# Kernel tuning notes

Measured on AMD Instinct MI355X. Metric: run time of the kernel, lower is better.

The kernel has to match this reference:

```python
import jax, jax.numpy as jnp
import numpy as np

B, S, H = 1, 1024, 2048
E, I, TOP_K = 64, 768, 8


def setup_inputs() -> dict:
    key = jax.random.key(0)
    k1, k2, k3, k4, k5 = jax.random.split(key, 5)
    std = 0.02
    return {
        "hidden_states": jax.random.normal(k1, (B, S, H), dtype=jnp.float32),
        "router_w": jax.random.normal(k2, (E, H), dtype=jnp.float32) * std,
        "gate_w": jax.random.normal(k3, (E, I, H), dtype=jnp.float32) * std,
        "up_w": jax.random.normal(k4, (E, I, H), dtype=jnp.float32) * std,
        "down_w": jax.random.normal(k5, (E, H, I), dtype=jnp.float32) * std,
    }


def reference(hidden_states, router_w, gate_w, up_w, down_w):
    b, s, h = hidden_states.shape
    x = hidden_states.reshape(-1, h)                     # [T, H]
    T = x.shape[0]

    # Router: softmax in fp32, top-k, renormalize (matches torch source).
    logits = x @ router_w.T                              # [T, E]
    probs = jax.nn.softmax(logits.astype(jnp.float32), axis=-1)
    topk_w, topk_idx = jax.lax.top_k(probs, TOP_K)       # [T, K]
    topk_w = topk_w / jnp.sum(topk_w, axis=-1, keepdims=True)
    topk_w = topk_w.astype(hidden_states.dtype)

    # Dense combine weights: zero for unselected experts. [T, E]
    tok = jnp.arange(T)[:, None]
    combine = jnp.zeros((T, E), dtype=hidden_states.dtype).at[tok, topk_idx].add(topk_w)

    # Scan over experts: SwiGLU MLP on all tokens, weighted-accumulate.
    # Tokens with zero combine weight contribute nothing (same math as the
    # gather/scatter loop in the torch source).
    def body(acc, p):
        gw, uw, dw, cw = p                                # [I,H],[I,H],[H,I],[T]
        hidden = jax.nn.silu(x @ gw.T) * (x @ uw.T)       # [T, I]
        out = hidden @ dw.T                               # [T, H]
        return acc + cw[:, None] * out, None

    init = jnp.zeros_like(x)
    final, _ = jax.lax.scan(body, init, (gate_w, up_w, down_w, combine.T))
    return final.reshape(b, s, h)
```

## Files before the change

kernel.cpp:

```cpp
#include <hip/hip_runtime.h>

#define T_TOK 1024
#define HD    2048
#define NE    64
#define ID    768
#define TOPK  8

typedef __bf16 bf16x8 __attribute__((ext_vector_type(8)));
typedef float  f32x4  __attribute__((ext_vector_type(4)));

#define LGKM0  asm volatile("s_waitcnt lgkmcnt(0)" ::: "memory")
#define VMC(N) asm volatile("s_waitcnt vmcnt(" N ")" ::: "memory")
#define BAR()  __builtin_amdgcn_s_barrier()
#define SCHED0 __builtin_amdgcn_sched_barrier(0)
#define FENCE  asm volatile("" ::: "memory")

__device__ __forceinline__ void load_lds16(const void* src, void* lds) {
  __builtin_amdgcn_global_load_lds(
      (const __attribute__((address_space(1))) void*)src,
      (__attribute__((address_space(3))) void*)lds, 16, 0, 0);
}

__device__ __forceinline__ bf16x8 cvt8(f32x4 a, f32x4 b) {
  bf16x8 r;
  #pragma unroll
  for (int j = 0; j < 4; ++j) { r[j] = (__bf16)a[j]; r[j + 4] = (__bf16)b[j]; }
  return r;
}

__global__ __launch_bounds__(256) void router_kernel(
    const float* __restrict__ x, const float* __restrict__ rw,
    unsigned short* __restrict__ xb_u, float* __restrict__ tw,
    int* __restrict__ counts, int* __restrict__ lists)
{
  __shared__ float  sx[HD];
  __shared__ double slog[NE];
  const int t = blockIdx.x;
  const int tid = threadIdx.x;
  __bf16* xb = (__bf16*)xb_u;

  for (int i = tid; i < HD; i += 256) {
    float v = x[(size_t)t * HD + i];
    sx[i] = v;
    xb[(size_t)t * HD + i] = (__bf16)v;
  }
  __syncthreads();

  const int e = tid >> 2, p = tid & 3;
  const float* rwrow = rw + (size_t)e * HD;
  double acc = 0.0;
  for (int k = p; k < HD; k += 4)
    acc += (double)sx[k] * (double)rwrow[k];
  acc += __shfl_xor(acc, 1, 64);
  acc += __shfl_xor(acc, 2, 64);
  if (p == 0) slog[e] = acc;
  __syncthreads();

  if (tid < 64) {
    double v = slog[tid];
    double selv = -1e300; int seli = 0; double gmax = 0.0;
    #pragma unroll
    for (int k = 0; k < TOPK; ++k) {
      double bv = v; int bi = tid;
      #pragma unroll
      for (int off = 32; off >= 1; off >>= 1) {
        double ov = __shfl_xor(bv, off, 64);
        int    oi = __shfl_xor(bi, off, 64);
        if (ov > bv || (ov == bv && oi < bi)) { bv = ov; bi = oi; }
      }
      if (k == 0) gmax = bv;
      if (tid == k) { selv = bv; seli = bi; }
      if (tid == bi) v = -1e300;
    }
    double e_ = (tid < TOPK) ? exp(selv - gmax) : 0.0;
    double s = e_;
    #pragma unroll
    for (int off = 32; off >= 1; off >>= 1) s += __shfl_xor(s, off, 64);
    if (tid < TOPK) {
      int slot = t * TOPK + tid;
      tw[slot] = (float)(e_ / s);
      int pos = atomicAdd(&counts[seli], 1);
      lists[seli * T_TOK + pos] = slot;
    }
  }
}

__global__ __launch_bounds__(512, 2) void gemm1_kernel(
    const unsigned short* __restrict__ xb_u,
    const float* __restrict__ gw, const float* __restrict__ uw,
    const int* __restrict__ counts, const int* __restrict__ lists,
    unsigned short* __restrict__ hb_u)
{
  __shared__ __bf16 sA[2][24576];
  __shared__ int    sSlot[192];

  const char* xbp = (const char*)xb_u;
  __bf16* hb = (__bf16*)hb_u;
  char* sAc = (char*)&sA[0][0];

  const int wg  = blockIdx.x;
  const int idx = wg >> 3;
  const int e   = (wg & 7) * 8 + idx / 12;
  const int n0  = (idx % 12) * 64;
  const int tid = threadIdx.x, wid = tid >> 6, lane = tid & 63;
  const int n_e = counts[e];
  const int isu = wid >> 2;

  const char* wlane = (const char*)(isu ? uw : gw)
      + ((size_t)e * ID + n0 + (wid & 3) * 16 + (lane & 15)) * (size_t)(HD * 4)
      + (size_t)(lane >> 4) * 32;

#define ISSUE_A1(BUFB, KC)                                                      \
  { char* dst_ = sAc + (BUFB) * 49152 + wid * 6144;                             \
    _Pragma("unroll") for (int j = 0; j < 6; ++j)                               \
      load_lds16(aAddr[j] + (KC) * 256, dst_ + j * 1024); }                     \
  FENCE;

#define ISSUE_W1(NXT, KC)                                                       \
  _Pragma("unroll") for (int p = 0; p < 8; ++p)                                 \
    NXT[p] = *(const f32x4*)(wlane + (size_t)(KC) * 512 + (p >> 1) * 128 + (p & 1) * 16); \
  FENCE;

#define COMP1(CUR, BUFB)                                                        \
  { const char* rb_ = sAc + (BUFB) * 49152;                                     \
    bf16x8 bf_[4];                                                              \
    _Pragma("unroll") for (int ks = 0; ks < 4; ++ks)                            \
      bf_[ks] = cvt8(CUR[2 * ks], CUR[2 * ks + 1]);                             \
    _Pragma("unroll") for (int ks = 0; ks < 4; ++ks) {                          \
      const int K_ = ks * 4 + (lane >> 4);                                      \
      _Pragma("unroll") for (int g = 0; g < 12; ++g) if (g * 16 < rem) {        \
        const int tok_ = g * 16 + (lane & 15);                                  \
        bf16x8 aF_ = *(const bf16x8*)(rb_ + tok_ * 256 + ((K_ ^ (tok_ & 7)) << 4)); \
        acc[g] = __builtin_amdgcn_mfma_f32_16x16x32_bf16(aF_, bf_[ks], acc[g], 0, 0, 0); } } }

#define STEP1(KC, CUR, NXT)                                                     \
  ISSUE_A1(((KC) + 1) & 1, (KC) + 1)                                            \
  ISSUE_W1(NXT, (KC) + 1)                                                       \
  COMP1(CUR, (KC) & 1)                                                          \
  LGKM0; SCHED0; VMC("8"); BAR();

  for (int m0 = 0; m0 < n_e; m0 += 192) {
    __syncthreads();
    if (tid < 192) sSlot[tid] = (m0 + tid < n_e) ? lists[e * T_TOK + m0 + tid] : 0;
    __syncthreads();
    const int rem = (n_e - m0 < 192) ? (n_e - m0) : 192;

    const char* aAddr[6];
    #pragma unroll
    for (int j = 0; j < 6; ++j) {
      int tok = wid * 24 + j * 4 + (lane >> 4);
      int sl = sSlot[tok];
      aAddr[j] = xbp + (size_t)(sl >> 3) * 4096 + (((lane & 15) ^ (tok & 7)) << 4);
    }

    f32x4 acc[12];
    #pragma unroll
    for (int g = 0; g < 12; ++g) acc[g] = (f32x4){0.f, 0.f, 0.f, 0.f};
    f32x4 wA[8], wB[8];

    ISSUE_A1(0, 0)
    ISSUE_W1(wA, 0)
    VMC("8"); BAR();

    #pragma unroll 1
    for (int it = 0; it < 7; ++it) {
      STEP1(2 * it,     wA, wB)
      STEP1(2 * it + 1, wB, wA)
    }
    STEP1(14, wA, wB)
    COMP1(wB, 1)

    if (isu) {
      #pragma unroll
      for (int g = 0; g < 12; ++g) if (g * 16 < rem)
        #pragma unroll
        for (int j = 0; j < 4; ++j) {
          int tok = g * 16 + (lane >> 4) * 4 + j;
          int cl = (wid & 3) * 16 + (lane & 15);
          *(float*)(sAc + tok * 256 + ((cl ^ ((tok & 3) << 4)) << 2)) = acc[g][j];
        }
    }
    __syncthreads();
    if (!isu) {
      #pragma unroll
      for (int g = 0; g < 12; ++g) if (g * 16 < rem)
        #pragma unroll
        for (int j = 0; j < 4; ++j) {
          int tok = g * 16 + (lane >> 4) * 4 + j;
          if (tok < rem) {
            int cl = (wid & 3) * 16 + (lane & 15);
            float uv = *(const float*)(sAc + tok * 256 + ((cl ^ ((tok & 3) << 4)) << 2));
            float gv = acc[g][j];
            int s = sSlot[tok];
            float hv = (gv / (1.0f + expf(-gv))) * uv;
            hb[(size_t)s * ID + (size_t)(n0 + cl)] = (__bf16)hv;
          }
        }
    }
    __syncthreads();
  }
#undef STEP1
#undef COMP1
#undef ISSUE_W1
#undef ISSUE_A1
}

__global__ __launch_bounds__(512, 2) void gemm2_kernel(
    const unsigned short* __restrict__ hb_u,
    const float* __restrict__ dw,
    const int* __restrict__ counts, const int* __restrict__ lists,
    const float* __restrict__ tw,
    float* __restrict__ out)
{
  __shared__ __bf16 sA[2][24576];
  __shared__ int    sSlot[192];

  const char* hbp = (const char*)hb_u;
  char* sAc = (char*)&sA[0][0];

  const int wg  = blockIdx.x;
  const int idx = wg >> 3;
  const int e   = (wg & 7) * 8 + idx / 16;
  const int n0  = (idx % 16) * 128;
  const int tid = threadIdx.x, wid = tid >> 6, lane = tid & 63;
  const int n_e = counts[e];

  const char* wlane = (const char*)dw
      + ((size_t)e * HD + n0 + wid * 16 + (lane & 15)) * (size_t)(ID * 4)
      + (size_t)(lane >> 4) * 32;

#define ISSUE_A2(BUFB, KC)                                                      \
  { char* dst_ = sAc + (BUFB) * 49152 + wid * 6144;                             \
    _Pragma("unroll") for (int j = 0; j < 6; ++j)                               \
      load_lds16(aAddr[j] + (KC) * 256, dst_ + j * 1024); }                     \
  FENCE;

#define ISSUE_W2(NXT, KC)                                                       \
  _Pragma("unroll") for (int p = 0; p < 8; ++p)                                 \
    NXT[p] = *(const f32x4*)(wlane + (size_t)(KC) * 512 + (p >> 1) * 128 + (p & 1) * 16); \
  FENCE;

#define COMP2(CUR, BUFB)                                                        \
  { const char* rb_ = sAc + (BUFB) * 49152;                                     \
    bf16x8 bf_[4];                                                              \
    _Pragma("unroll") for (int ks = 0; ks < 4; ++ks)                            \
      bf_[ks] = cvt8(CUR[2 * ks], CUR[2 * ks + 1]);                             \
    _Pragma("unroll") for (int ks = 0; ks < 4; ++ks) {                          \
      const int K_ = ks * 4 + (lane >> 4);                                      \
      _Pragma("unroll") for (int g = 0; g < 12; ++g) if (g * 16 < rem) {        \
        const int tok_ = g * 16 + (lane & 15);                                  \
        bf16x8 aF_ = *(const bf16x8*)(rb_ + tok_ * 256 + ((K_ ^ (tok_ & 7)) << 4)); \
        acc[g] = __builtin_amdgcn_mfma_f32_16x16x32_bf16(aF_, bf_[ks], acc[g], 0, 0, 0); } } }

#define STEP2(KC, CUR, NXT)                                                     \
  ISSUE_A2(((KC) + 1) & 1, (KC) + 1)                                            \
  ISSUE_W2(NXT, (KC) + 1)                                                       \
  COMP2(CUR, (KC) & 1)                                                          \
  LGKM0; SCHED0; VMC("8"); BAR();

  for (int m0 = 0; m0 < n_e; m0 += 192) {
    __syncthreads();
    if (tid < 192) sSlot[tid] = (m0 + tid < n_e) ? lists[e * T_TOK + m0 + tid] : 0;
    __syncthreads();
    const int rem = (n_e - m0 < 192) ? (n_e - m0) : 192;

    const char* aAddr[6];
    #pragma unroll
    for (int j = 0; j < 6; ++j) {
      int tok = wid * 24 + j * 4 + (lane >> 4);
      int sl = sSlot[tok];
      aAddr[j] = hbp + (size_t)sl * 1536 + (((lane & 15) ^ (tok & 7)) << 4);
    }

    f32x4 acc[12];
    #pragma unroll
    for (int g = 0; g < 12; ++g) acc[g] = (f32x4){0.f, 0.f, 0.f, 0.f};
    f32x4 wA[8], wB[8];

    ISSUE_A2(0, 0)
    ISSUE_W2(wA, 0)
    VMC("8"); BAR();

    #pragma unroll 1
    for (int it = 0; it < 2; ++it) {
      STEP2(2 * it,     wA, wB)
      STEP2(2 * it + 1, wB, wA)
    }
    STEP2(4, wA, wB)
    COMP2(wB, 1)

    #pragma unroll
    for (int g = 0; g < 12; ++g) if (g * 16 < rem)
      #pragma unroll
      for (int j = 0; j < 4; ++j) {
        int tok = g * 16 + (lane >> 4) * 4 + j;
        if (tok < rem) {
          int s = sSlot[tok];
          float w = tw[s];
          atomicAdd(out + (size_t)(s >> 3) * HD + (size_t)(n0 + wid * 16 + (lane & 15)),
                    w * acc[g][j]);
        }
      }
  }
#undef STEP2
#undef COMP2
#undef ISSUE_W2
#undef ISSUE_A2
}

extern "C" void kernel_launch(void* const* d_in, const int* in_sizes, int n_in,
                              void* d_out, int out_size, void* d_ws, size_t ws_size,
                              hipStream_t stream) {
  const float* x  = (const float*)d_in[0];
  const float* rw = (const float*)d_in[1];
  const float* gw = (const float*)d_in[2];
  const float* uw = (const float*)d_in[3];
  const float* dw = (const float*)d_in[4];
  float* out = (float*)d_out;

  char* ws = (char*)d_ws;
  const size_t XB_OFF  = 0;
  const size_t TW_OFF  = XB_OFF + (size_t)T_TOK * HD * 2;
  const size_t CNT_OFF = TW_OFF + (size_t)T_TOK * TOPK * 4;
  const size_t LST_OFF = CNT_OFF + 256;
  const size_t HB_OFF  = LST_OFF + (size_t)NE * T_TOK * 4;

  unsigned short* xb  = (unsigned short*)(ws + XB_OFF);
  float*          tw  = (float*)(ws + TW_OFF);
  int*            cnt = (int*)(ws + CNT_OFF);
  int*            lst = (int*)(ws + LST_OFF);
  unsigned short* hb  = (unsigned short*)(ws + HB_OFF);

  hipMemsetAsync(cnt, 0, 256, stream);
  hipMemsetAsync(d_out, 0, (size_t)T_TOK * HD * sizeof(float), stream);

  router_kernel<<<T_TOK, 256, 0, stream>>>(x, rw, xb, tw, cnt, lst);
  gemm1_kernel<<<768, 512, 0, stream>>>(xb, gw, uw, cnt, lst, hb);
  gemm2_kernel<<<1024, 512, 0, stream>>>(hb, dw, cnt, lst, tw, out);
}
```

Baseline: 516.9 us.

## Halve K-chunk per pipeline stage to cut LDS and registers for higher occupancy

Both expert GEMM kernels now process a 64-wide K chunk per step instead of 128, halving the double-buffered LDS tile and the per-lane weight register buffers. Launch bounds are raised from 2 to 4 blocks per CU to exploit the smaller footprint. The K loop runs twice as many steps, each with its own barrier and waitcnt, and the final step drains with vmcnt(0). This trades more synchronisation per unit of work for more resident waves to hide global load latency.

```diff
diff --git a/kernel.cpp b/kernel.cpp
--- a/kernel.cpp
+++ b/kernel.cpp
@@ -9,7 +9,6 @@
 typedef __bf16 bf16x8 __attribute__((ext_vector_type(8)));
 typedef float  f32x4  __attribute__((ext_vector_type(4)));
 
-#define LGKM0  asm volatile("s_waitcnt lgkmcnt(0)" ::: "memory")
 #define VMC(N) asm volatile("s_waitcnt vmcnt(" N ")" ::: "memory")
 #define BAR()  __builtin_amdgcn_s_barrier()
 #define SCHED0 __builtin_amdgcn_sched_barrier(0)
@@ -85,13 +84,13 @@
   }
 }
 
-__global__ __launch_bounds__(512, 2) void gemm1_kernel(
+__global__ __launch_bounds__(512, 4) void gemm1_kernel(
     const unsigned short* __restrict__ xb_u,
     const float* __restrict__ gw, const float* __restrict__ uw,
     const int* __restrict__ counts, const int* __restrict__ lists,
     unsigned short* __restrict__ hb_u)
 {
-  __shared__ __bf16 sA[2][24576];
+  __shared__ __bf16 sA[2][12288];
   __shared__ int    sSlot[192];
 
   const char* xbp = (const char*)xb_u;
@@ -110,34 +109,35 @@
       + ((size_t)e * ID + n0 + (wid & 3) * 16 + (lane & 15)) * (size_t)(HD * 4)
       + (size_t)(lane >> 4) * 32;
 
-#define ISSUE_A1(BUFB, KC)                                                      \
-  { char* dst_ = sAc + (BUFB) * 49152 + wid * 6144;                             \
-    _Pragma("unroll") for (int j = 0; j < 6; ++j)                               \
-      load_lds16(aAddr[j] + (KC) * 256, dst_ + j * 1024); }                     \
-  FENCE;
-
-#define ISSUE_W1(NXT, KC)                                                       \
-  _Pragma("unroll") for (int p = 0; p < 8; ++p)                                 \
-    NXT[p] = *(const f32x4*)(wlane + (size_t)(KC) * 512 + (p >> 1) * 128 + (p & 1) * 16); \
-  FENCE;
-
-#define COMP1(CUR, BUFB)                                                        \
-  { const char* rb_ = sAc + (BUFB) * 49152;                                     \
-    bf16x8 bf_[4];                                                              \
-    _Pragma("unroll") for (int ks = 0; ks < 4; ++ks)                            \
-      bf_[ks] = cvt8(CUR[2 * ks], CUR[2 * ks + 1]);                             \
-    _Pragma("unroll") for (int ks = 0; ks < 4; ++ks) {                          \
-      const int K_ = ks * 4 + (lane >> 4);                                      \
+#define STEP1(BUFC, CUR, NXT, KN, DOI)                                          \
+  {                                                                             \
+    if (DOI) {                                                                  \
+      char* d_ = sAc + (1 - (BUFC)) * 24576 + wid * 3072;                       \
+      load_lds16(aA0 + (size_t)(KN) * 128, d_);                                 \
+      load_lds16(aA1 + (size_t)(KN) * 128, d_ + 1024);                          \
+      load_lds16(aA2 + (size_t)(KN) * 128, d_ + 2048);                          \
+      NXT[0] = *(const f32x4*)(wlane + (size_t)(KN) * 256);                     \
+      NXT[1] = *(const f32x4*)(wlane + (size_t)(KN) * 256 + 16);                \
+      NXT[2] = *(const f32x4*)(wlane + (size_t)(KN) * 256 + 128);               \
+      NXT[3] = *(const f32x4*)(wlane + (size_t)(KN) * 256 + 144);               \
+    }                                                                           \
+    FENCE;                                                                      \
+    {                                                                           \
+      const char* rb_ = sAc + (BUFC) * 24576;                                   \
+      bf16x8 bw0_ = cvt8(CUR[0], CUR[1]);                                       \
+      bf16x8 bw1_ = cvt8(CUR[2], CUR[3]);                                       \
+      const int c0_ = (lane >> 4), c1_ = 4 + (lane >> 4);                       \
       _Pragma("unroll") for (int g = 0; g < 12; ++g) if (g * 16 < rem) {        \
         const int tok_ = g * 16 + (lane & 15);                                  \
-        bf16x8 aF_ = *(const bf16x8*)(rb_ + tok_ * 256 + ((K_ ^ (tok_ & 7)) << 4)); \
-        acc[g] = __builtin_amdgcn_mfma_f32_16x16x32_bf16(aF_, bf_[ks], acc[g], 0, 0, 0); } } }
-
-#define STEP1(KC, CUR, NXT)                                                     \
-  ISSUE_A1(((KC) + 1) & 1, (KC) + 1)                                            \
-  ISSUE_W1(NXT, (KC) + 1)                                                       \
-  COMP1(CUR, (KC) & 1)                                                          \
-  LGKM0; SCHED0; VMC("8"); BAR();
+        bf16x8 a0_ = *(const bf16x8*)(rb_ + tok_ * 128 + ((c0_ ^ (tok_ & 7)) << 4)); \
+        acc[g] = __builtin_amdgcn_mfma_f32_16x16x32_bf16(a0_, bw0_, acc[g], 0, 0, 0); \
+        bf16x8 a1_ = *(const bf16x8*)(rb_ + tok_ * 128 + ((c1_ ^ (tok_ & 7)) << 4)); \
+        acc[g] = __builtin_amdgcn_mfma_f32_16x16x32_bf16(a1_, bw1_, acc[g], 0, 0, 0); \
+      }                                                                         \
+    }                                                                           \
+    if (DOI) { VMC("4"); } else { VMC("0"); }                                   \
+    BAR(); SCHED0;                                                              \
+  }
 
   for (int m0 = 0; m0 < n_e; m0 += 192) {
     __syncthreads();
@@ -145,30 +145,37 @@
     __syncthreads();
     const int rem = (n_e - m0 < 192) ? (n_e - m0) : 192;
 
-    const char* aAddr[6];
-    #pragma unroll
-    for (int j = 0; j < 6; ++j) {
-      int tok = wid * 24 + j * 4 + (lane >> 4);
-      int sl = sSlot[tok];
-      aAddr[j] = xbp + (size_t)(sl >> 3) * 4096 + (((lane & 15) ^ (tok & 7)) << 4);
-    }
+    const int r0 = wid * 24 + (lane >> 3);
+    const int r1 = r0 + 8, r2 = r0 + 16;
+    const char* aA0 = xbp + (size_t)(sSlot[r0] >> 3) * 4096 + (((lane & 7) ^ (r0 & 7)) << 4);
+    const char* aA1 = xbp + (size_t)(sSlot[r1] >> 3) * 4096 + (((lane & 7) ^ (r1 & 7)) << 4);
+    const char* aA2 = xbp + (size_t)(sSlot[r2] >> 3) * 4096 + (((lane & 7) ^ (r2 & 7)) << 4);
 
     f32x4 acc[12];
     #pragma unroll
     for (int g = 0; g < 12; ++g) acc[g] = (f32x4){0.f, 0.f, 0.f, 0.f};
-    f32x4 wA[8], wB[8];
-
-    ISSUE_A1(0, 0)
-    ISSUE_W1(wA, 0)
-    VMC("8"); BAR();
+    f32x4 wA[4], wB[4];
+
+    {
+      char* d_ = sAc + wid * 3072;
+      load_lds16(aA0, d_);
+      load_lds16(aA1, d_ + 1024);
+      load_lds16(aA2, d_ + 2048);
+      wA[0] = *(const f32x4*)(wlane);
+      wA[1] = *(const f32x4*)(wlane + 16);
+      wA[2] = *(const f32x4*)(wlane + 128);
+      wA[3] = *(const f32x4*)(wlane + 144);
+    }
+    FENCE;
+    VMC("4"); BAR(); SCHED0;
 
     #pragma unroll 1
-    for (int it = 0; it < 7; ++it) {
-      STEP1(2 * it,     wA, wB)
-      STEP1(2 * it + 1, wB, wA)
-    }
-    STEP1(14, wA, wB)
-    COMP1(wB, 1)
+    for (int it = 0; it < 15; ++it) {
+      STEP1(0, wA, wB, 2 * it + 1, 1)
+      STEP1(1, wB, wA, 2 * it + 2, 1)
+    }
+    STEP1(0, wA, wB, 31, 1)
+    STEP1(1, wB, wA, 0, 0)
 
     if (isu) {
       #pragma unroll
@@ -200,19 +207,16 @@
     __syncthreads();
   }
 #undef STEP1
-#undef COMP1
-#undef ISSUE_W1
-#undef ISSUE_A1
-}
-
-__global__ __launch_bounds__(512, 2) void gemm2_kernel(
+}
+
+__global__ __launch_bounds__(512, 4) void gemm2_kernel(
     const unsigned short* __restrict__ hb_u,
     const float* __restrict__ dw,
     const int* __restrict__ counts, const int* __restrict__ lists,
     const float* __restrict__ tw,
     float* __restrict__ out)
 {
-  __shared__ __bf16 sA[2][24576];
+  __shared__ __bf16 sA[2][12288];
   __shared__ int    sSlot[192];
 
   const char* hbp = (const char*)hb_u;
@@ -229,34 +233,35 @@
       + ((size_t)e * HD + n0 + wid * 16 + (lane & 15)) * (size_t)(ID * 4)
       + (size_t)(lane >> 4) * 32;
 
-#define ISSUE_A2(BUFB, KC)                                                      \
-  { char* dst_ = sAc + (BUFB) * 49152 + wid * 6144;                             \
-    _Pragma("unroll") for (int j = 0; j < 6; ++j)                               \
-      load_lds16(aAddr[j] + (KC) * 256, dst_ + j * 1024); }                     \
-  FENCE;
-
-#define ISSUE_W2(NXT, KC)                                                       \
-  _Pragma("unroll") for (int p = 0; p < 8; ++p)                                 \
-    NXT[p] = *(const f32x4*)(wlane + (size_t)(KC) * 512 + (p >> 1) * 128 + (p & 1) * 16); \
-  FENCE;
-
-#define COMP2(CUR, BUFB)                                                        \
-  { const char* rb_ = sAc + (BUFB) * 49152;                                     \
-    bf16x8 bf_[4];                                                              \
-    _Pragma("unroll") for (int ks = 0; ks < 4; ++ks)                            \
-      bf_[ks] = cvt8(CUR[2 * ks], CUR[2 * ks + 1]);                             \
-    _Pragma("unroll") for (int ks = 0; ks < 4; ++ks) {                          \
-      const int K_ = ks * 4 + (lane >> 4);                                      \
+#define STEP2(BUFC, CUR, NXT, KN, DOI)                                          \
+  {                                                                             \
+    if (DOI) {                                                                  \
+      char* d_ = sAc + (1 - (BUFC)) * 24576 + wid * 3072;                       \
+      load_lds16(aA0 + (size_t)(KN) * 128, d_);                                 \
+      load_lds16(aA1 + (size_t)(KN) * 128, d_ + 1024);                          \
+      load_lds16(aA2 + (size_t)(KN) * 128, d_ + 2048);                          \
+      NXT[0] = *(const f32x4*)(wlane + (size_t)(KN) * 256);                     \
+      NXT[1] = *(const f32x4*)(wlane + (size_t)(KN) * 256 + 16);                \
+      NXT[2] = *(const f32x4*)(wlane + (size_t)(KN) * 256 + 128);               \
+      NXT[3] = *(const f32x4*)(wlane + (size_t)(KN) * 256 + 144);               \
+    }                                                                           \
+    FENCE;                                                                      \
+    {                                                                           \
+      const char* rb_ = sAc + (BUFC) * 24576;                                   \
+      bf16x8 bw0_ = cvt8(CUR[0], CUR[1]);                                       \
+      bf16x8 bw1_ = cvt8(CUR[2], CUR[3]);                                       \
+      const int c0_ = (lane >> 4), c1_ = 4 + (lane >> 4);                       \
       _Pragma("unroll") for (int g = 0; g < 12; ++g) if (g * 16 < rem) {        \
         const int tok_ = g * 16 + (lane & 15);                                  \
-        bf16x8 aF_ = *(const bf16x8*)(rb_ + tok_ * 256 + ((K_ ^ (tok_ & 7)) << 4)); \
-        acc[g] = __builtin_amdgcn_mfma_f32_16x16x32_bf16(aF_, bf_[ks], acc[g], 0, 0, 0); } } }
-
-#define STEP2(KC, CUR, NXT)                                                     \
-  ISSUE_A2(((KC) + 1) & 1, (KC) + 1)                                            \
-  ISSUE_W2(NXT, (KC) + 1)                                                       \
-  COMP2(CUR, (KC) & 1)                                                          \
-  LGKM0; SCHED0; VMC("8"); BAR();
+        bf16x8 a0_ = *(const bf16x8*)(rb_ + tok_ * 128 + ((c0_ ^ (tok_ & 7)) << 4)); \
+        acc[g] = __builtin_amdgcn_mfma_f32_16x16x32_bf16(a0_, bw0_, acc[g], 0, 0, 0); \
+        bf16x8 a1_ = *(const bf16x8*)(rb_ + tok_ * 128 + ((c1_ ^ (tok_ & 7)) << 4)); \
+        acc[g] = __builtin_amdgcn_mfma_f32_16x16x32_bf16(a1_, bw1_, acc[g], 0, 0, 0); \
+      }                                                                         \
+    }                                                                           \
+    if (DOI) { VMC("4"); } else { VMC("0"); }                                   \
+    BAR(); SCHED0;                                                              \
+  }
 
   for (int m0 = 0; m0 < n_e; m0 += 192) {
     __syncthreads();
@@ -264,30 +269,37 @@
     __syncthreads();
     const int rem = (n_e - m0 < 192) ? (n_e - m0) : 192;
 
-    const char* aAddr[6];
-    #pragma unroll
-    for (int j = 0; j < 6; ++j) {
-      int tok = wid * 24 + j * 4 + (lane >> 4);
-      int sl = sSlot[tok];
-      aAddr[j] = hbp + (size_t)sl * 1536 + (((lane & 15) ^ (tok & 7)) << 4);
-    }
+    const int r0 = wid * 24 + (lane >> 3);
+    const int r1 = r0 + 8, r2 = r0 + 16;
+    const char* aA0 = hbp + (size_t)sSlot[r0] * 1536 + (((lane & 7) ^ (r0 & 7)) << 4);
+    const char* aA1 = hbp + (size_t)sSlot[r1] * 1536 + (((lane & 7) ^ (r1 & 7)) << 4);
+    const char* aA2 = hbp + (size_t)sSlot[r2] * 1536 + (((lane & 7) ^ (r2 & 7)) << 4);
 
     f32x4 acc[12];
     #pragma unroll
     for (int g = 0; g < 12; ++g) acc[g] = (f32x4){0.f, 0.f, 0.f, 0.f};
-    f32x4 wA[8], wB[8];
-
-    ISSUE_A2(0, 0)
-    ISSUE_W2(wA, 0)
-    VMC("8"); BAR();
+    f32x4 wA[4], wB[4];
+
+    {
+      char* d_ = sAc + wid * 3072;
+      load_lds16(aA0, d_);
+      load_lds16(aA1, d_ + 1024);
+      load_lds16(aA2, d_ + 2048);
+      wA[0] = *(const f32x4*)(wlane);
+      wA[1] = *(const f32x4*)(wlane + 16);
+      wA[2] = *(const f32x4*)(wlane + 128);
+      wA[3] = *(const f32x4*)(wlane + 144);
+    }
+    FENCE;
+    VMC("4"); BAR(); SCHED0;
 
     #pragma unroll 1
-    for (int it = 0; it < 2; ++it) {
-      STEP2(2 * it,     wA, wB)
-      STEP2(2 * it + 1, wB, wA)
-    }
-    STEP2(4, wA, wB)
-    COMP2(wB, 1)
+    for (int it = 0; it < 5; ++it) {
+      STEP2(0, wA, wB, 2 * it + 1, 1)
+      STEP2(1, wB, wA, 2 * it + 2, 1)
+    }
+    STEP2(0, wA, wB, 11, 1)
+    STEP2(1, wB, wA, 0, 0)
 
     #pragma unroll
     for (int g = 0; g < 12; ++g) if (g * 16 < rem)
@@ -303,9 +315,6 @@
       }
   }
 #undef STEP2
-#undef COMP2
-#undef ISSUE_W2
-#undef ISSUE_A2
 }
 
 extern "C" void kernel_launch(void* const* d_in, const int* in_sizes, int n_in,
```

Measured after the change: 597.2 us. 1.16x slower.
